# Optimization experiments

Measured on AMD Instinct MI355X. Metric: run time of the kernel, lower is better.

Reference implementation:

```python
import jax, jax.numpy as jnp
import numpy as np

NUM_TILES = 32
N_HEAD = 4
D_MODEL = 256


def build_key_indices(n):
    # Mirrors the torch __init__ loop: row+column neighbors of token i on an n x n grid.
    key_indices = []
    for i in range(n * n):
        idx = []
        start = i // n
        end = i % n
        for j in range(n):
            idx.append(start * n + j)
            idx.append(end + n * j)
        idx.remove(i)  # i appears twice; one occurrence remains, matching torch
        key_indices.append(sorted(idx))
    return np.asarray(key_indices, dtype=np.int32)  # [T, 2n-1]


def setup_inputs() -> dict:
    key = jax.random.key(0)
    ks = jax.random.split(key, 5)
    B, T, D = 4, NUM_TILES ** 2, D_MODEL
    K = 2 * NUM_TILES - 1
    x = jax.random.normal(ks[0], (B, T, D), jnp.float32)
    scale = 1.0 / np.sqrt(D)
    Wq = jax.random.normal(ks[1], (D, D), jnp.float32) * scale  # [out, in] torch layout
    Wk = jax.random.normal(ks[2], (D, D), jnp.float32) * scale
    Wv = jax.random.normal(ks[3], (D, D), jnp.float32) * scale
    lim = np.sqrt(6.0 / (T + K))  # xavier_uniform
    wbias = jax.random.uniform(ks[4], (T, K), jnp.float32, -lim, lim)
    key_indices = jnp.asarray(build_key_indices(NUM_TILES))
    return {"x": x, "Wq": Wq, "Wk": Wk, "Wv": Wv, "wbias": wbias,
            "key_indices": key_indices}


def reference(x, Wq, Wk, Wv, wbias, key_indices):
    B, T, D = x.shape
    H = N_HEAD
    d = D // H
    # projections (torch Linear: x @ W.T), split heads -> [B,H,T,d]
    q = (x @ Wq.T).reshape(B, T, H, d).transpose(0, 2, 1, 3)
    k = (x @ Wk.T).reshape(B, T, H, d).transpose(0, 2, 1, 3)
    v = (x @ Wv.T).reshape(B, T, H, d).transpose(0, 2, 1, 3)

    ew = jnp.exp(wbias)          # [T, K]
    ek = jnp.exp(k)              # [B,H,T,d]
    kv = ek * v                  # [B,H,T,d]

    kv_g = kv[:, :, key_indices, :]   # gather -> [B,H,T,K,d]
    ek_g = ek[:, :, key_indices, :]   # gather -> [B,H,T,K,d]

    num = jnp.einsum('tk,bhtkd->bhtd', ew, kv_g)
    den = jnp.einsum('tk,bhtkd->bhtd', ew, ek_g)
    weighted = num / den

    out = jax.nn.sigmoid(q) * weighted          # [B,H,T,d]
    return out.transpose(0, 2, 1, 3).reshape(B, T, D)
```

## Files before the change

kernel.cpp:

```cpp
#include <hip/hip_runtime.h>
#include <hip/hip_bf16.h>
#include <math.h>

#define TT   1024
#define DD   256
#define KN   63
#define BB   4
#define MM   (BB * TT)
#define NW   768

typedef short bf16x8 __attribute__((ext_vector_type(8)));
typedef float f32x4  __attribute__((ext_vector_type(4)));

__device__ __forceinline__ unsigned short bf16bits(float f) {
    __hip_bfloat16 h = __float2bfloat16(f);
    return *reinterpret_cast<unsigned short*>(&h);
}
__device__ __forceinline__ float bf16tof(unsigned short u) {
    __hip_bfloat16 h;
    *reinterpret_cast<unsigned short*>(&h) = u;
    return __bfloat162float(h);
}

__global__ __launch_bounds__(256) void prep_kernel(
    const float* __restrict__ x,  const float* __restrict__ Wq,
    const float* __restrict__ Wk, const float* __restrict__ Wv,
    const float* __restrict__ wbias, const int* __restrict__ kidx,
    __hip_bfloat16* __restrict__ xh, __hip_bfloat16* __restrict__ xl,
    __hip_bfloat16* __restrict__ Wh, __hip_bfloat16* __restrict__ Wl,
    float* __restrict__ Aw, float* __restrict__ Bw)
{
    const int bid = blockIdx.x, tid = threadIdx.x;
    if (bid < 1024) {
        const int e = bid * 1024 + tid * 4;
        float4 v = *reinterpret_cast<const float4*>(&x[e]);
        float vf[4] = {v.x, v.y, v.z, v.w};
        ushort4 hh, ll;
        unsigned short* hp = &hh.x;
        unsigned short* lp = &ll.x;
        #pragma unroll
        for (int i = 0; i < 4; ++i) {
            unsigned short h = bf16bits(vf[i]);
            hp[i] = h;
            lp[i] = bf16bits(vf[i] - bf16tof(h));
        }
        *reinterpret_cast<ushort4*>(xh + e) = hh;
        *reinterpret_cast<ushort4*>(xl + e) = ll;
    } else if (bid < 1216) {
        const int e = (bid - 1024) * 1024 + tid * 4;
        const int zz = e >> 16;
        const float* __restrict__ Ws = (zz == 0) ? Wq : (zz == 1) ? Wk : Wv;
        const int off = e & 65535;
        float4 v = *reinterpret_cast<const float4*>(&Ws[off]);
        float vf[4] = {v.x, v.y, v.z, v.w};
        ushort4 hh, ll;
        unsigned short* hp = &hh.x;
        unsigned short* lp = &ll.x;
        #pragma unroll
        for (int i = 0; i < 4; ++i) {
            unsigned short h = bf16bits(vf[i]);
            hp[i] = h;
            lp[i] = bf16bits(vf[i] - bf16tof(h));
        }
        *reinterpret_cast<ushort4*>(Wh + e) = hh;
        *reinterpret_cast<ushort4*>(Wl + e) = ll;
    } else {
        __shared__ float wbuf[4][64];
        const int wv = tid >> 6, lane = tid & 63;
        const int t = (bid - 1216) * 4 + wv;
        wbuf[wv][lane] = 0.0f;
        __syncthreads();
        if (lane < KN) {
            const float w  = __expf(wbias[t * KN + lane]);
            const int  idx = kidx[t * KN + lane];
            const int  ir = idx >> 5, ic = idx & 31;
            const int  rr = t >> 5;
            if (ir == rr) wbuf[wv][ic] = w;
            else          wbuf[wv][32 + ir] = w;
        }
        __syncthreads();
        if (lane < 32) Aw[t * 32 + lane] = wbuf[wv][lane];
        else           Bw[t * 32 + (lane - 32)] = wbuf[wv][lane - 32 + 32];
    }
}

__device__ __forceinline__ void stage_tile(const __hip_bfloat16* __restrict__ src,
                                           char* __restrict__ lds, int tid)
{
    #pragma unroll
    for (int i = 0; i < 2; ++i) {
        const int slot = tid + i * 256;
        const int row = slot >> 2;
        const int ks  = slot & 3;
        int4 v = *reinterpret_cast<const int4*>(src + (size_t)row * DD + ks * 8);
        *reinterpret_cast<int4*>(lds + row * 64 + ((ks ^ ((row >> 1) & 3)) << 4)) = v;
    }
}

__global__ __launch_bounds__(256) void proj_mfma(
    const __hip_bfloat16* __restrict__ xh, const __hip_bfloat16* __restrict__ xl,
    const __hip_bfloat16* __restrict__ Wh, const __hip_bfloat16* __restrict__ Wl,
    float* __restrict__ P, float* __restrict__ E, float* __restrict__ V)
{
    __shared__ char lds[32768];
    const int tid = threadIdx.x;
    const int lane = tid & 63, wave = tid >> 6;
    const int wr = wave >> 1, wc = wave & 1;
    const int m0 = blockIdx.x * 128;
    const int ny = blockIdx.y;
    const int n0 = ny * 128;

    f32x4 acc[4][4];
    #pragma unroll
    for (int i = 0; i < 4; ++i)
        #pragma unroll
        for (int j = 0; j < 4; ++j) acc[i][j] = (f32x4)0.0f;

    const int kg = lane >> 4, li = lane & 15;

    for (int kt = 0; kt < 8; ++kt) {
        const int k0 = kt * 32;
        stage_tile(xh + (size_t)m0 * DD + k0, lds,         tid);
        stage_tile(xl + (size_t)m0 * DD + k0, lds + 8192,  tid);
        stage_tile(Wh + (size_t)n0 * DD + k0, lds + 16384, tid);
        stage_tile(Wl + (size_t)n0 * DD + k0, lds + 24576, tid);
        __syncthreads();

        bf16x8 bh[4], bl[4];
        #pragma unroll
        for (int fn = 0; fn < 4; ++fn) {
            const int r   = wc * 64 + fn * 16 + li;
            const int off = r * 64 + ((kg ^ ((r >> 1) & 3)) << 4);
            bh[fn] = *reinterpret_cast<const bf16x8*>(lds + 16384 + off);
            bl[fn] = *reinterpret_cast<const bf16x8*>(lds + 24576 + off);
        }
        #pragma unroll
        for (int fm = 0; fm < 4; ++fm) {
            const int r   = wr * 64 + fm * 16 + li;
            const int off = r * 64 + ((kg ^ ((r >> 1) & 3)) << 4);
            bf16x8 ah = *reinterpret_cast<const bf16x8*>(lds + off);
            bf16x8 al = *reinterpret_cast<const bf16x8*>(lds + 8192 + off);
            #pragma unroll
            for (int fn = 0; fn < 4; ++fn) {
                acc[fm][fn] = __builtin_amdgcn_mfma_f32_16x16x32_bf16(ah, bh[fn], acc[fm][fn], 0, 0, 0);
                acc[fm][fn] = __builtin_amdgcn_mfma_f32_16x16x32_bf16(ah, bl[fn], acc[fm][fn], 0, 0, 0);
                acc[fm][fn] = __builtin_amdgcn_mfma_f32_16x16x32_bf16(al, bh[fn], acc[fm][fn], 0, 0, 0);
            }
        }
        __syncthreads();
    }

    const int region = ny >> 1;
    float* __restrict__ ob = (region == 0) ? P : (region == 1) ? E : V;
    const int ncol0 = (ny & 1) * 128;
    const int lj = (lane >> 4) << 2;
    #pragma unroll
    for (int fm = 0; fm < 4; ++fm) {
        #pragma unroll
        for (int fn = 0; fn < 4; ++fn) {
            const int mb = m0 + wr * 64 + fm * 16 + lj;
            const int cc = ncol0 + wc * 64 + fn * 16 + li;
            #pragma unroll
            for (int j = 0; j < 4; ++j) {
                float v0 = acc[fm][fn][j];
                if (region == 0)      v0 = 1.0f / (1.0f + __expf(-v0));
                else if (region == 1) v0 = __expf(v0);
                ob[(size_t)(mb + j) * DD + cc] = v0;
            }
        }
    }
}

__global__ __launch_bounds__(256) void rowpass(
    const float* __restrict__ E, const float* __restrict__ V,
    const float* __restrict__ Aw, float* __restrict__ Nout, float* __restrict__ Dout)
{
    __shared__ float Et[32][132], Vt[32][132], At[32][36];
    const int bid = blockIdx.x, tid = threadIdx.x;
    const int dh = bid & 1, r = (bid >> 1) & 31, b = bid >> 6;
    const size_t base = ((size_t)(b * TT + r * 32)) * DD + dh * 128;

    #pragma unroll
    for (int i = 0; i < 4; ++i) {
        const int slot = tid + i * 256;
        const int row = slot >> 5, c4 = (slot & 31) * 4;
        *reinterpret_cast<f32x4*>(&Et[row][c4]) =
            *reinterpret_cast<const f32x4*>(&E[base + (size_t)row * DD + c4]);
        *reinterpret_cast<f32x4*>(&Vt[row][c4]) =
            *reinterpret_cast<const f32x4*>(&V[base + (size_t)row * DD + c4]);
    }
    {
        const int c = tid >> 3, j4 = (tid & 7) * 4;
        *reinterpret_cast<f32x4*>(&At[c][j4]) =
            *reinterpret_cast<const f32x4*>(&Aw[(size_t)(r * 32 + c) * 32 + j4]);
    }
    __syncthreads();

    const int dq = tid & 31, cg = tid >> 5;
    f32x4 num[4], den[4];
    #pragma unroll
    for (int ci = 0; ci < 4; ++ci) { num[ci] = (f32x4)0.0f; den[ci] = (f32x4)0.0f; }

    for (int j = 0; j < 32; ++j) {
        f32x4 e = *reinterpret_cast<const f32x4*>(&Et[j][dq * 4]);
        f32x4 v = *reinterpret_cast<const f32x4*>(&Vt[j][dq * 4]);
        f32x4 ev = e * v;
        #pragma unroll
        for (int ci = 0; ci < 4; ++ci) {
            const float w = At[cg * 4 + ci][j];
            den[ci] += e * w;
            num[ci] += ev * w;
        }
    }
    #pragma unroll
    for (int ci = 0; ci < 4; ++ci) {
        const size_t o = ((size_t)(b * TT + r * 32 + cg * 4 + ci)) * DD + dh * 128 + dq * 4;
        *reinterpret_cast<f32x4*>(&Nout[o]) = num[ci];
        *reinterpret_cast<f32x4*>(&Dout[o]) = den[ci];
    }
}

__global__ __launch_bounds__(256) void colpass(
    const float* __restrict__ E, const float* __restrict__ V,
    const float* __restrict__ Bw, const float* __restrict__ P,
    const float* __restrict__ Drow, float* __restrict__ out)
{
    __shared__ float Et[32][132], Vt[32][132], Bt[32][36];
    const int bid = blockIdx.x, tid = threadIdx.x;
    const int dh = bid & 1, c = (bid >> 1) & 31, b = bid >> 6;

    #pragma unroll
    for (int i = 0; i < 4; ++i) {
        const int slot = tid + i * 256;
        const int j = slot >> 5, c4 = (slot & 31) * 4;
        const size_t g = ((size_t)(b * TT + j * 32 + c)) * DD + dh * 128 + c4;
        *reinterpret_cast<f32x4*>(&Et[j][c4]) = *reinterpret_cast<const f32x4*>(&E[g]);
        *reinterpret_cast<f32x4*>(&Vt[j][c4]) = *reinterpret_cast<const f32x4*>(&V[g]);
    }
    {
        const int rr = tid >> 3, j4 = (tid & 7) * 4;
        *reinterpret_cast<f32x4*>(&Bt[rr][j4]) =
            *reinterpret_cast<const f32x4*>(&Bw[(size_t)(rr * 32 + c) * 32 + j4]);
    }
    __syncthreads();

    const int dq = tid & 31, rg = tid >> 5;
    f32x4 num[4], den[4];
    #pragma unroll
    for (int ri = 0; ri < 4; ++ri) { num[ri] = (f32x4)0.0f; den[ri] = (f32x4)0.0f; }

    for (int j = 0; j < 32; ++j) {
        f32x4 e = *reinterpret_cast<const f32x4*>(&Et[j][dq * 4]);
        f32x4 v = *reinterpret_cast<const f32x4*>(&Vt[j][dq * 4]);
        f32x4 ev = e * v;
        #pragma unroll
        for (int ri = 0; ri < 4; ++ri) {
            const float w = Bt[rg * 4 + ri][j];
            den[ri] += e * w;
            num[ri] += ev * w;
        }
    }
    #pragma unroll
    for (int ri = 0; ri < 4; ++ri) {
        const size_t o = ((size_t)(b * TT + (rg * 4 + ri) * 32 + c)) * DD + dh * 128 + dq * 4;
        f32x4 nr = *reinterpret_cast<const f32x4*>(&out[o]);
        f32x4 dr = *reinterpret_cast<const f32x4*>(&Drow[o]);
        f32x4 p  = *reinterpret_cast<const f32x4*>(&P[o]);
        f32x4 res = p * (num[ri] + nr) / (den[ri] + dr);
        *reinterpret_cast<f32x4*>(&out[o]) = res;
    }
}

extern "C" void kernel_launch(void* const* d_in, const int* in_sizes, int n_in,
                              void* d_out, int out_size, void* d_ws, size_t ws_size,
                              hipStream_t stream) {
    const float* x     = (const float*)d_in[0];
    const float* Wq    = (const float*)d_in[1];
    const float* Wk    = (const float*)d_in[2];
    const float* Wv    = (const float*)d_in[3];
    const float* wbias = (const float*)d_in[4];
    const int*   kidx  = (const int*)d_in[5];

    float* P  = (float*)d_ws;
    float* E  = P + 1048576;
    float* V  = E + 1048576;
    float* Aw = V + 1048576;
    float* Bw = Aw + 32768;
    __hip_bfloat16* xh = (__hip_bfloat16*)(Bw + 32768);
    __hip_bfloat16* xl = xh + 1048576;
    __hip_bfloat16* Wh = xl + 1048576;
    __hip_bfloat16* Wl = Wh + 196608;
    float* Dbuf = (float*)xh;

    prep_kernel<<<1472, 256, 0, stream>>>(x, Wq, Wk, Wv, wbias, kidx,
                                          xh, xl, Wh, Wl, Aw, Bw);
    proj_mfma<<<dim3(32, 6), 256, 0, stream>>>(xh, xl, Wh, Wl, P, E, V);
    rowpass<<<256, 256, 0, stream>>>(E, V, Aw, (float*)d_out, Dbuf);
    colpass<<<256, 256, 0, stream>>>(E, V, Bw, P, Dbuf, (float*)d_out);
}
```

Baseline: 102.7 us.

## Fuse bf16 split into projection GEMM and build weight tables inside row/col passes

Removes the separate prep kernel. The fp32-to-bf16 hi/lo split of x and W now happens while tiles are staged into LDS in the MFMA projection, and the exp(wbias) neighbour tables are scattered directly into shared memory inside rowpass and colpass. The GEMM tile shrinks to 64x64 with a 64x12 grid to raise block count. This cuts one launch and the global round trip of the split buffers, at the cost of redundant split work across blocks and scattered, divide-based table construction in each pass.

Result: slower. 104.9 us (+2.1%).

```diff
diff --git a/kernel.cpp b/kernel.cpp
--- a/kernel.cpp
+++ b/kernel.cpp
@@ -7,7 +7,6 @@
 #define KN   63
 #define BB   4
 #define MM   (BB * TT)
-#define NW   768
 
 typedef short bf16x8 __attribute__((ext_vector_type(8)));
 typedef float f32x4  __attribute__((ext_vector_type(4)));
@@ -21,127 +20,79 @@
     *reinterpret_cast<unsigned short*>(&h) = u;
     return __bfloat162float(h);
 }
-
-__global__ __launch_bounds__(256) void prep_kernel(
+__device__ __forceinline__ void split4(float4 v, ushort4& h, ushort4& l) {
+    float vf[4] = {v.x, v.y, v.z, v.w};
+    unsigned short* hp = &h.x;
+    unsigned short* lp = &l.x;
+    #pragma unroll
+    for (int i = 0; i < 4; ++i) {
+        unsigned short b = bf16bits(vf[i]);
+        hp[i] = b;
+        lp[i] = bf16bits(vf[i] - bf16tof(b));
+    }
+}
+
+__global__ __launch_bounds__(256) void proj_mfma(
     const float* __restrict__ x,  const float* __restrict__ Wq,
     const float* __restrict__ Wk, const float* __restrict__ Wv,
-    const float* __restrict__ wbias, const int* __restrict__ kidx,
-    __hip_bfloat16* __restrict__ xh, __hip_bfloat16* __restrict__ xl,
-    __hip_bfloat16* __restrict__ Wh, __hip_bfloat16* __restrict__ Wl,
-    float* __restrict__ Aw, float* __restrict__ Bw)
-{
-    const int bid = blockIdx.x, tid = threadIdx.x;
-    if (bid < 1024) {
-        const int e = bid * 1024 + tid * 4;
-        float4 v = *reinterpret_cast<const float4*>(&x[e]);
-        float vf[4] = {v.x, v.y, v.z, v.w};
-        ushort4 hh, ll;
-        unsigned short* hp = &hh.x;
-        unsigned short* lp = &ll.x;
-        #pragma unroll
-        for (int i = 0; i < 4; ++i) {
-            unsigned short h = bf16bits(vf[i]);
-            hp[i] = h;
-            lp[i] = bf16bits(vf[i] - bf16tof(h));
-        }
-        *reinterpret_cast<ushort4*>(xh + e) = hh;
-        *reinterpret_cast<ushort4*>(xl + e) = ll;
-    } else if (bid < 1216) {
-        const int e = (bid - 1024) * 1024 + tid * 4;
-        const int zz = e >> 16;
-        const float* __restrict__ Ws = (zz == 0) ? Wq : (zz == 1) ? Wk : Wv;
-        const int off = e & 65535;
-        float4 v = *reinterpret_cast<const float4*>(&Ws[off]);
-        float vf[4] = {v.x, v.y, v.z, v.w};
-        ushort4 hh, ll;
-        unsigned short* hp = &hh.x;
-        unsigned short* lp = &ll.x;
-        #pragma unroll
-        for (int i = 0; i < 4; ++i) {
-            unsigned short h = bf16bits(vf[i]);
-            hp[i] = h;
-            lp[i] = bf16bits(vf[i] - bf16tof(h));
-        }
-        *reinterpret_cast<ushort4*>(Wh + e) = hh;
-        *reinterpret_cast<ushort4*>(Wl + e) = ll;
-    } else {
-        __shared__ float wbuf[4][64];
-        const int wv = tid >> 6, lane = tid & 63;
-        const int t = (bid - 1216) * 4 + wv;
-        wbuf[wv][lane] = 0.0f;
-        __syncthreads();
-        if (lane < KN) {
-            const float w  = __expf(wbias[t * KN + lane]);
-            const int  idx = kidx[t * KN + lane];
-            const int  ir = idx >> 5, ic = idx & 31;
-            const int  rr = t >> 5;
-            if (ir == rr) wbuf[wv][ic] = w;
-            else          wbuf[wv][32 + ir] = w;
-        }
-        __syncthreads();
-        if (lane < 32) Aw[t * 32 + lane] = wbuf[wv][lane];
-        else           Bw[t * 32 + (lane - 32)] = wbuf[wv][lane - 32 + 32];
-    }
-}
-
-__device__ __forceinline__ void stage_tile(const __hip_bfloat16* __restrict__ src,
-                                           char* __restrict__ lds, int tid)
-{
-    #pragma unroll
-    for (int i = 0; i < 2; ++i) {
-        const int slot = tid + i * 256;
-        const int row = slot >> 2;
-        const int ks  = slot & 3;
-        int4 v = *reinterpret_cast<const int4*>(src + (size_t)row * DD + ks * 8);
-        *reinterpret_cast<int4*>(lds + row * 64 + ((ks ^ ((row >> 1) & 3)) << 4)) = v;
-    }
-}
-
-__global__ __launch_bounds__(256) void proj_mfma(
-    const __hip_bfloat16* __restrict__ xh, const __hip_bfloat16* __restrict__ xl,
-    const __hip_bfloat16* __restrict__ Wh, const __hip_bfloat16* __restrict__ Wl,
     float* __restrict__ P, float* __restrict__ E, float* __restrict__ V)
 {
-    __shared__ char lds[32768];
-    const int tid = threadIdx.x;
+    __shared__ char lds[16384];
+    const int tid  = threadIdx.x;
     const int lane = tid & 63, wave = tid >> 6;
     const int wr = wave >> 1, wc = wave & 1;
-    const int m0 = blockIdx.x * 128;
+    const int m0 = blockIdx.x * 64;
     const int ny = blockIdx.y;
-    const int n0 = ny * 128;
-
-    f32x4 acc[4][4];
-    #pragma unroll
-    for (int i = 0; i < 4; ++i)
-        #pragma unroll
-        for (int j = 0; j < 4; ++j) acc[i][j] = (f32x4)0.0f;
-
-    const int kg = lane >> 4, li = lane & 15;
+    const int region = ny >> 2;
+    const float* __restrict__ Ws = (region == 0) ? Wq : (region == 1) ? Wk : Wv;
+    const int w0 = (ny & 3) * 64;
+
+    f32x4 acc[2][2];
+    #pragma unroll
+    for (int i = 0; i < 2; ++i)
+        #pragma unroll
+        for (int j = 0; j < 2; ++j) acc[i][j] = (f32x4)0.0f;
+
+    const int li = lane & 15, kg = lane >> 4;
 
     for (int kt = 0; kt < 8; ++kt) {
         const int k0 = kt * 32;
-        stage_tile(xh + (size_t)m0 * DD + k0, lds,         tid);
-        stage_tile(xl + (size_t)m0 * DD + k0, lds + 8192,  tid);
-        stage_tile(Wh + (size_t)n0 * DD + k0, lds + 16384, tid);
-        stage_tile(Wl + (size_t)n0 * DD + k0, lds + 24576, tid);
+        #pragma unroll
+        for (int i = 0; i < 2; ++i) {
+            const int s   = tid + i * 256;
+            const int row = s >> 3;
+            const int q   = s & 7;
+            float4 a = *reinterpret_cast<const float4*>(
+                &x[(size_t)(m0 + row) * DD + k0 + q * 4]);
+            float4 b = *reinterpret_cast<const float4*>(
+                &Ws[(size_t)(w0 + row) * DD + k0 + q * 4]);
+            ushort4 xh_, xl_, wh_, wl_;
+            split4(a, xh_, xl_);
+            split4(b, wh_, wl_);
+            const int off = row * 64 + ((((q >> 1)) ^ (row & 3)) << 4) + (q & 1) * 8;
+            *reinterpret_cast<ushort4*>(lds + off)         = xh_;
+            *reinterpret_cast<ushort4*>(lds + 4096  + off) = xl_;
+            *reinterpret_cast<ushort4*>(lds + 8192  + off) = wh_;
+            *reinterpret_cast<ushort4*>(lds + 12288 + off) = wl_;
+        }
         __syncthreads();
 
-        bf16x8 bh[4], bl[4];
-        #pragma unroll
-        for (int fn = 0; fn < 4; ++fn) {
-            const int r   = wc * 64 + fn * 16 + li;
-            const int off = r * 64 + ((kg ^ ((r >> 1) & 3)) << 4);
-            bh[fn] = *reinterpret_cast<const bf16x8*>(lds + 16384 + off);
-            bl[fn] = *reinterpret_cast<const bf16x8*>(lds + 24576 + off);
-        }
-        #pragma unroll
-        for (int fm = 0; fm < 4; ++fm) {
-            const int r   = wr * 64 + fm * 16 + li;
-            const int off = r * 64 + ((kg ^ ((r >> 1) & 3)) << 4);
+        bf16x8 bh[2], bl[2];
+        #pragma unroll
+        for (int fn = 0; fn < 2; ++fn) {
+            const int r   = wc * 32 + fn * 16 + li;
+            const int off = r * 64 + ((kg ^ (r & 3)) << 4);
+            bh[fn] = *reinterpret_cast<const bf16x8*>(lds + 8192  + off);
+            bl[fn] = *reinterpret_cast<const bf16x8*>(lds + 12288 + off);
+        }
+        #pragma unroll
+        for (int fm = 0; fm < 2; ++fm) {
+            const int r   = wr * 32 + fm * 16 + li;
+            const int off = r * 64 + ((kg ^ (r & 3)) << 4);
             bf16x8 ah = *reinterpret_cast<const bf16x8*>(lds + off);
-            bf16x8 al = *reinterpret_cast<const bf16x8*>(lds + 8192 + off);
+            bf16x8 al = *reinterpret_cast<const bf16x8*>(lds + 4096 + off);
             #pragma unroll
-            for (int fn = 0; fn < 4; ++fn) {
+            for (int fn = 0; fn < 2; ++fn) {
                 acc[fm][fn] = __builtin_amdgcn_mfma_f32_16x16x32_bf16(ah, bh[fn], acc[fm][fn], 0, 0, 0);
                 acc[fm][fn] = __builtin_amdgcn_mfma_f32_16x16x32_bf16(ah, bl[fn], acc[fm][fn], 0, 0, 0);
                 acc[fm][fn] = __builtin_amdgcn_mfma_f32_16x16x32_bf16(al, bh[fn], acc[fm][fn], 0, 0, 0);
@@ -150,22 +101,20 @@
         __syncthreads();
     }
 
-    const int region = ny >> 1;
     float* __restrict__ ob = (region == 0) ? P : (region == 1) ? E : V;
-    const int ncol0 = (ny & 1) * 128;
-    const int lj = (lane >> 4) << 2;
-    #pragma unroll
-    for (int fm = 0; fm < 4; ++fm) {
-        #pragma unroll
-        for (int fn = 0; fn < 4; ++fn) {
-            const int mb = m0 + wr * 64 + fm * 16 + lj;
-            const int cc = ncol0 + wc * 64 + fn * 16 + li;
+    const int colbase = (ny & 3) * 64 + wc * 32;
+    #pragma unroll
+    for (int fm = 0; fm < 2; ++fm) {
+        #pragma unroll
+        for (int fn = 0; fn < 2; ++fn) {
+            const int rb = m0 + wr * 32 + fm * 16 + kg * 4;
+            const int cc = colbase + fn * 16 + li;
             #pragma unroll
             for (int j = 0; j < 4; ++j) {
                 float v0 = acc[fm][fn][j];
                 if (region == 0)      v0 = 1.0f / (1.0f + __expf(-v0));
                 else if (region == 1) v0 = __expf(v0);
-                ob[(size_t)(mb + j) * DD + cc] = v0;
+                ob[(size_t)(rb + j) * DD + cc] = v0;
             }
         }
     }
@@ -173,9 +122,10 @@
 
 __global__ __launch_bounds__(256) void rowpass(
     const float* __restrict__ E, const float* __restrict__ V,
-    const float* __restrict__ Aw, float* __restrict__ Nout, float* __restrict__ Dout)
+    const float* __restrict__ wbias, const int* __restrict__ kidx,
+    float* __restrict__ Nout, float* __restrict__ Dout)
 {
-    __shared__ float Et[32][132], Vt[32][132], At[32][36];
+    __shared__ float Et[32][132], Vt[32][132], At[32][33];
     const int bid = blockIdx.x, tid = threadIdx.x;
     const int dh = bid & 1, r = (bid >> 1) & 31, b = bid >> 6;
     const size_t base = ((size_t)(b * TT + r * 32)) * DD + dh * 128;
@@ -189,10 +139,11 @@
         *reinterpret_cast<f32x4*>(&Vt[row][c4]) =
             *reinterpret_cast<const f32x4*>(&V[base + (size_t)row * DD + c4]);
     }
-    {
-        const int c = tid >> 3, j4 = (tid & 7) * 4;
-        *reinterpret_cast<f32x4*>(&At[c][j4]) =
-            *reinterpret_cast<const f32x4*>(&Aw[(size_t)(r * 32 + c) * 32 + j4]);
+    for (int e = tid; e < 32 * KN; e += 256) {
+        const int c = e / KN, k = e - c * KN;
+        const int t = r * 32 + c;
+        const int idx = kidx[t * KN + k];
+        if ((idx >> 5) == r) At[c][idx & 31] = __expf(wbias[t * KN + k]);
     }
     __syncthreads();
 
@@ -222,10 +173,11 @@
 
 __global__ __launch_bounds__(256) void colpass(
     const float* __restrict__ E, const float* __restrict__ V,
-    const float* __restrict__ Bw, const float* __restrict__ P,
-    const float* __restrict__ Drow, float* __restrict__ out)
+    const float* __restrict__ wbias, const int* __restrict__ kidx,
+    const float* __restrict__ P, const float* __restrict__ Drow,
+    float* __restrict__ out)
 {
-    __shared__ float Et[32][132], Vt[32][132], Bt[32][36];
+    __shared__ float Et[32][132], Vt[32][132], Bt[32][33];
     const int bid = blockIdx.x, tid = threadIdx.x;
     const int dh = bid & 1, c = (bid >> 1) & 31, b = bid >> 6;
 
@@ -237,10 +189,15 @@
         *reinterpret_cast<f32x4*>(&Et[j][c4]) = *reinterpret_cast<const f32x4*>(&E[g]);
         *reinterpret_cast<f32x4*>(&Vt[j][c4]) = *reinterpret_cast<const f32x4*>(&V[g]);
     }
-    {
-        const int rr = tid >> 3, j4 = (tid & 7) * 4;
-        *reinterpret_cast<f32x4*>(&Bt[rr][j4]) =
-            *reinterpret_cast<const f32x4*>(&Bw[(size_t)(rr * 32 + c) * 32 + j4]);
+    for (int e = tid; e < 32 * 33; e += 256) (&Bt[0][0])[e] = 0.0f;
+    __syncthreads();
+
+    for (int e = tid; e < 32 * KN; e += 256) {
+        const int rp = e / KN, k = e - rp * KN;
+        const int t = rp * 32 + c;
+        const int idx = kidx[t * KN + k];
+        const int ir = idx >> 5;
+        if (ir != rp) Bt[rp][ir] = __expf(wbias[t * KN + k]);
     }
     __syncthreads();
 
@@ -281,20 +238,12 @@
     const float* wbias = (const float*)d_in[4];
     const int*   kidx  = (const int*)d_in[5];
 
-    float* P  = (float*)d_ws;
-    float* E  = P + 1048576;
-    float* V  = E + 1048576;
-    float* Aw = V + 1048576;
-    float* Bw = Aw + 32768;
-    __hip_bfloat16* xh = (__hip_bfloat16*)(Bw + 32768);
-    __hip_bfloat16* xl = xh + 1048576;
-    __hip_bfloat16* Wh = xl + 1048576;
-    __hip_bfloat16* Wl = Wh + 196608;
-    float* Dbuf = (float*)xh;
-
-    prep_kernel<<<1472, 256, 0, stream>>>(x, Wq, Wk, Wv, wbias, kidx,
-                                          xh, xl, Wh, Wl, Aw, Bw);
-    proj_mfma<<<dim3(32, 6), 256, 0, stream>>>(xh, xl, Wh, Wl, P, E, V);
-    rowpass<<<256, 256, 0, stream>>>(E, V, Aw, (float*)d_out, Dbuf);
-    colpass<<<256, 256, 0, stream>>>(E, V, Bw, P, Dbuf, (float*)d_out);
-}
+    float* P    = (float*)d_ws;
+    float* E    = P + 1048576;
+    float* V    = E + 1048576;
+    float* Dbuf = V + 1048576;
+
+    proj_mfma<<<dim3(64, 12), 256, 0, stream>>>(x, Wq, Wk, Wv, P, E, V);
+    rowpass<<<256, 256, 0, stream>>>(E, V, wbias, kidx, (float*)d_out, Dbuf);
+    colpass<<<256, 256, 0, stream>>>(E, V, wbias, kidx, P, Dbuf, (float*)d_out);
+}
```
